# Performance work log

Measured on AMD Instinct MI355X. Metric: run time of the kernel, lower is better.

## Reference

```python
import jax, jax.numpy as jnp
import numpy as np

B, T, D, H = 64, 2048, 128, 256
EPS = 1e-5


def setup_inputs() -> dict:
    key = jax.random.key(0)
    ks = jax.random.split(key, 20)
    s_d = 1.0 / np.sqrt(D)
    s_h = 1.0 / np.sqrt(H)
    s_2h = 1.0 / np.sqrt(2 * H)
    u = lambda k, shape, s: jax.random.uniform(k, shape, jnp.float32, -s, s)
    return {
        "x": jax.random.normal(ks[0], (B, T, D), jnp.float32),
        # gate input projections, stored (in, out)
        "Wi": u(ks[1], (D, H), s_d), "bi": u(ks[2], (H,), s_d),
        "Wf": u(ks[3], (D, H), s_d), "bf": u(ks[4], (H,), s_d),
        "Wc": u(ks[5], (D, H), s_d), "bc": u(ks[6], (H,), s_d),
        "Wo": u(ks[7], (D, H), s_d), "bo": u(ks[8], (H,), s_d),
        # recurrent projections (no bias)
        "Ui": u(ks[9], (H, H), s_h), "Uf": u(ks[10], (H, H), s_h),
        "Uc": u(ks[11], (H, H), s_h), "Uo": u(ks[12], (H, H), s_h),
        # KAN MLP: H -> 2H -> H
        "K1": u(ks[13], (H, 2 * H), s_h), "kb1": u(ks[14], (2 * H,), s_h),
        "K2": u(ks[15], (2 * H, H), s_2h), "kb2": u(ks[16], (H,), s_2h),
        # LayerNorm
        "gamma": jnp.ones((H,), jnp.float32), "beta": jnp.zeros((H,), jnp.float32),
    }


def _layernorm(h, gamma, beta):
    mu = jnp.mean(h, axis=-1, keepdims=True)
    var = jnp.mean(jnp.square(h - mu), axis=-1, keepdims=True)
    return (h - mu) * jax.lax.rsqrt(var + EPS) * gamma + beta


def _forward(x, Wi, bi, Wf, bf, Wc, bc, Wo, bo, Ui, Uf, Uc, Uo, K1, kb1, K2, kb2, gamma, beta):
    # Precompute input projections for all timesteps: (B,T,H) -> scan over T
    xi = jnp.einsum("btd,dh->bth", x, Wi) + bi
    xf = jnp.einsum("btd,dh->bth", x, Wf) + bf
    xc = jnp.einsum("btd,dh->bth", x, Wc) + bc
    xo = jnp.einsum("btd,dh->bth", x, Wo) + bo
    xs = jnp.stack([xi, xf, xc, xo], axis=0).transpose(2, 0, 1, 3)  # (T,4,B,H)

    h0 = jnp.zeros((x.shape[0], Wi.shape[1]), x.dtype)
    c0 = jnp.zeros_like(h0)

    def step(carry, xt):
        h, c = carry
        xi_t, xf_t, xc_t, xo_t = xt[0], xt[1], xt[2], xt[3]
        i_t = jax.nn.sigmoid(xi_t + h @ Ui)
        f_t = jax.nn.sigmoid(xf_t + h @ Uf)
        c_tilde = jnp.tanh(xc_t + h @ Uc)
        o_t = jax.nn.sigmoid(xo_t + h @ Uo)
        c = f_t * c + i_t * c_tilde
        c_tr = jnp.tanh(c @ K1 + kb1) @ K2 + kb2  # KAN transform
        h = o_t * jnp.tanh(c_tr)
        h = _layernorm(h, gamma, beta)  # dropout is identity in eval mode
        return (h, c), h

    (h, c), ys = jax.lax.scan(step, (h0, c0), xs)
    output = ys.transpose(1, 0, 2)  # (B,T,H)
    return output, h, c


def reference(x, Wi, bi, Wf, bf, Wc, bc, Wo, bo, Ui, Uf, Uc, Uo, K1, kb1, K2, kb2, gamma, beta):
    return _forward(x, Wi, bi, Wf, bf, Wc, bc, Wo, bo, Ui, Uf, Uc, Uo, K1, kb1, K2, kb2, gamma, beta)
```

## Files before the change

### kernel.cpp

```cpp
#include <hip/hip_runtime.h>

#define B 64
#define T 2048
#define D 128
#define H 256
#define H2 512
#define NP 4
#define CHUNK 8

#define ROW_U64 1536
#define WS_NEEDED ((size_t)B * ROW_U64 * 8)
#define SPIN_LIM (1 << 20)

__device__ __forceinline__ float sigmoid_f(float x) { return 1.f / (1.f + __expf(-x)); }
__device__ __forceinline__ float tanh_f(float x) {
    float e = __expf(2.f * x);
    return 1.f - 2.f / (e + 1.f);
}
__device__ __forceinline__ unsigned long long pack_tag(float v, unsigned int tag) {
    return ((unsigned long long)tag << 32) | (unsigned long long)__float_as_uint(v);
}
__device__ __forceinline__ float poll_tagged(const unsigned long long* __restrict__ ptr,
                                             unsigned int tag, bool& alive) {
    unsigned long long v;
    if (alive) {
        int cnt = 0;
        do {
            v = __hip_atomic_load(ptr, __ATOMIC_RELAXED, __HIP_MEMORY_SCOPE_AGENT);
            if ((unsigned int)(v >> 32) == tag)
                return __uint_as_float((unsigned int)v);
        } while (++cnt < SPIN_LIM);
        alive = false;
    }
    v = __hip_atomic_load(ptr, __ATOMIC_RELAXED, __HIP_MEMORY_SCOPE_AGENT);
    return __uint_as_float((unsigned int)v);
}

#define FMA4(A_, S_, W_) \
    A_.x = fmaf(S_, W_.x, A_.x); A_.y = fmaf(S_, W_.y, A_.y); \
    A_.z = fmaf(S_, W_.z, A_.z); A_.w = fmaf(S_, W_.w, A_.w);

__global__ __launch_bounds__(512, 2) void scan_kernel(
    const float* __restrict__ x,
    const float* __restrict__ Wi, const float* __restrict__ bi,
    const float* __restrict__ Wf, const float* __restrict__ bf,
    const float* __restrict__ Wc, const float* __restrict__ bc,
    const float* __restrict__ Wo, const float* __restrict__ bo,
    const float* __restrict__ Ui, const float* __restrict__ Uf,
    const float* __restrict__ Uc, const float* __restrict__ Uo,
    const float* __restrict__ K1, const float* __restrict__ kb1,
    const float* __restrict__ K2, const float* __restrict__ kb2,
    const float* __restrict__ gamma, const float* __restrict__ beta,
    float* __restrict__ out,
    unsigned long long* __restrict__ ws)
{
    const int bid = blockIdx.x;
    const int b   = bid >> 2;
    const int p   = bid & 3;
    const int tid = threadIdx.x;

    __shared__ float k2lds[128 * 256];
    __shared__ float xw[CHUNK][256];
    __shared__ float red[2048];
    __shared__ float hs[H], cs[H], os[H], us[H], ts[128];

    const int kq  = tid >> 6;
    const int grp = tid & 63;
    const int gG  = grp >> 4;
    const int jG  = (grp & 15) * 4;
    const int ks1 = ((tid >> 6) << 1) | ((tid >> 5) & 1);
    const int mg1 = tid & 31;

    const float* Ug = (gG == 0) ? Ui : (gG == 1) ? Uf : (gG == 2) ? Uc : Uo;
    const float* Wg = (gG == 0) ? Wi : (gG == 1) ? Wf : (gG == 2) ? Wc : Wo;

    float4 uw[32];
    #pragma unroll
    for (int k = 0; k < 32; ++k)
        uw[k] = *(const float4*)(Ug + (size_t)(kq * 32 + k) * H + p * 64 + jG);

    float4 k1w[16];
    #pragma unroll
    for (int k = 0; k < 16; ++k)
        k1w[k] = *(const float4*)(K1 + (size_t)(ks1 * 16 + k) * H2 + p * 128 + mg1 * 4);

    for (int idx = tid; idx < 128 * 64; idx += 512) {
        int k = idx >> 6, jg = (idx & 63) * 4;
        *(float4*)&k2lds[k * 256 + jg] = *(const float4*)(K2 + (size_t)(p * 128 + k) * H + jg);
    }

    float bcat = 0.f, kb1r = 0.f, kb2r = 0.f;
    float4 gam4, bet4;
    if (tid < 256) {
        const int g = tid >> 6, jj = tid & 63;
        const float* bp = (g == 0) ? bi : (g == 1) ? bf : (g == 2) ? bc : bo;
        bcat = bp[p * 64 + jj];
        kb2r = kb2[tid];
    }
    if (tid < 128) kb1r = kb1[p * 128 + tid];
    if (tid < 64) {
        gam4 = *(const float4*)(gamma + tid * 4);
        bet4 = *(const float4*)(beta + tid * 4);
    }

    if (tid < 256) hs[tid] = 0.f;
    float c_reg = 0.f;

    const float* xrow = x + (size_t)b * T * D;
    float* yb = out + (size_t)b * T * H;
    unsigned long long* rowp  = ws + (size_t)b * ROW_U64;
    unsigned long long* slotC = rowp;
    unsigned long long* slotO = rowp + 256;
    unsigned long long* slotH = rowp + 512;
    const int dqu = __builtin_amdgcn_readfirstlane(kq);

    bool alive = true;
    __syncthreads();

    for (int t = 0; t < T; ++t) {
        const int tt8 = t & (CHUNK - 1);
        const unsigned int seq = (unsigned int)(t + 1);

        if (tt8 == 0) {
            const float* Wp = Wg + p * 64 + jG;
            #pragma unroll
            for (int pass = 0; pass < 2; ++pass) {
                float4 acc[4];
                #pragma unroll
                for (int r = 0; r < 4; ++r) acc[r] = make_float4(0.f, 0.f, 0.f, 0.f);
                #pragma unroll 4
                for (int dd = 0; dd < 16; ++dd) {
                    const int d = dqu * 16 + dd;
                    float4 w = *(const float4*)(Wp + (size_t)d * H);
                    #pragma unroll
                    for (int r = 0; r < 4; ++r) {
                        float xv = xrow[(size_t)(t + pass * 4 + r) * D + d];
                        FMA4(acc[r], xv, w);
                    }
                }
                #pragma unroll
                for (int r = 0; r < 4; ++r) {
                    *(float4*)&red[kq * 256 + grp * 4] = acc[r];
                    __syncthreads();
                    if (tid < 256) {
                        float s = bcat;
                        #pragma unroll
                        for (int q = 0; q < 8; ++q) s += red[q * 256 + tid];
                        xw[pass * 4 + r][tid] = s;
                    }
                    __syncthreads();
                }
            }
        }

        {
            float4 a = make_float4(0.f, 0.f, 0.f, 0.f);
            #pragma unroll
            for (int k4 = 0; k4 < 8; ++k4) {
                float4 hv = *(const float4*)&hs[kq * 32 + k4 * 4];
                FMA4(a, hv.x, uw[k4 * 4 + 0]);
                FMA4(a, hv.y, uw[k4 * 4 + 1]);
                FMA4(a, hv.z, uw[k4 * 4 + 2]);
                FMA4(a, hv.w, uw[k4 * 4 + 3]);
            }
            *(float4*)&red[kq * 256 + grp * 4] = a;
        }
        __syncthreads();
        if (tid < 64) {
            const int j = tid;
            float si = xw[tt8][j],        sf = xw[tt8][64 + j],
                  sg = xw[tt8][128 + j],  so = xw[tt8][192 + j];
            #pragma unroll
            for (int q = 0; q < 8; ++q) {
                si += red[q * 256 + j];
                sf += red[q * 256 + 64 + j];
                sg += red[q * 256 + 128 + j];
                so += red[q * 256 + 192 + j];
            }
            float iv = sigmoid_f(si), fv = sigmoid_f(sf);
            float gv = tanh_f(sg),    ov = sigmoid_f(so);
            float c = fmaf(fv, c_reg, iv * gv);
            c_reg = c;
            cs[p * 64 + j] = c;
            os[p * 64 + j] = ov;
            __hip_atomic_store(slotC + p * 64 + j, pack_tag(c, seq),
                               __ATOMIC_RELAXED, __HIP_MEMORY_SCOPE_AGENT);
            __hip_atomic_store(slotO + p * 64 + j, pack_tag(ov, seq),
                               __ATOMIC_RELAXED, __HIP_MEMORY_SCOPE_AGENT);
        } else if (tid < 448) {
            const int idx = tid - 64;
            if (idx < 192) {
                const int q  = (p + 1 + (idx >> 6)) & 3;
                const int gj = q * 64 + (idx & 63);
                cs[gj] = poll_tagged(slotC + gj, seq, alive);
            } else {
                const int i2 = idx - 192;
                const int q  = (p + 1 + (i2 >> 6)) & 3;
                const int gj = q * 64 + (i2 & 63);
                os[gj] = poll_tagged(slotO + gj, seq, alive);
            }
        }
        __syncthreads();

        {
            float4 a = make_float4(0.f, 0.f, 0.f, 0.f);
            #pragma unroll
            for (int k4 = 0; k4 < 4; ++k4) {
                float4 cv = *(const float4*)&cs[ks1 * 16 + k4 * 4];
                FMA4(a, cv.x, k1w[k4 * 4 + 0]);
                FMA4(a, cv.y, k1w[k4 * 4 + 1]);
                FMA4(a, cv.z, k1w[k4 * 4 + 2]);
                FMA4(a, cv.w, k1w[k4 * 4 + 3]);
            }
            *(float4*)&red[ks1 * 128 + mg1 * 4] = a;
        }
        __syncthreads();
        if (tid < 128) {
            float s = kb1r;
            #pragma unroll
            for (int q = 0; q < 16; ++q) s += red[q * 128 + tid];
            ts[tid] = tanh_f(s);
        }
        __syncthreads();

        {
            float4 a = make_float4(0.f, 0.f, 0.f, 0.f);
            #pragma unroll
            for (int kk = 0; kk < 16; kk += 4) {
                float4 tv = *(const float4*)&ts[kq * 16 + kk];
                float4 w0 = *(const float4*)&k2lds[(kq * 16 + kk + 0) * 256 + grp * 4];
                float4 w1 = *(const float4*)&k2lds[(kq * 16 + kk + 1) * 256 + grp * 4];
                float4 w2 = *(const float4*)&k2lds[(kq * 16 + kk + 2) * 256 + grp * 4];
                float4 w3 = *(const float4*)&k2lds[(kq * 16 + kk + 3) * 256 + grp * 4];
                FMA4(a, tv.x, w0);
                FMA4(a, tv.y, w1);
                FMA4(a, tv.z, w2);
                FMA4(a, tv.w, w3);
            }
            *(float4*)&red[kq * 256 + grp * 4] = a;
        }
        __syncthreads();
        if (tid < 256) {
            float ph = 0.f;
            #pragma unroll
            for (int q = 0; q < 8; ++q) ph += red[q * 256 + tid];
            __hip_atomic_store(slotH + p * 256 + tid, pack_tag(ph, seq),
                               __ATOMIC_RELAXED, __HIP_MEMORY_SCOPE_AGENT);
            const unsigned long long* q1 = slotH + (((p + 1) & 3) << 8) + tid;
            const unsigned long long* q2 = slotH + (((p + 2) & 3) << 8) + tid;
            const unsigned long long* q3 = slotH + (((p + 3) & 3) << 8) + tid;
            unsigned long long v1 = 0, v2 = 0, v3 = 0;
            bool d1 = false, d2 = false, d3 = false;
            int cnt = 0;
            const int lim = alive ? SPIN_LIM : 2;
            while (true) {
                if (!d1) v1 = __hip_atomic_load(q1, __ATOMIC_RELAXED, __HIP_MEMORY_SCOPE_AGENT);
                if (!d2) v2 = __hip_atomic_load(q2, __ATOMIC_RELAXED, __HIP_MEMORY_SCOPE_AGENT);
                if (!d3) v3 = __hip_atomic_load(q3, __ATOMIC_RELAXED, __HIP_MEMORY_SCOPE_AGENT);
                d1 = d1 | ((unsigned int)(v1 >> 32) == seq);
                d2 = d2 | ((unsigned int)(v2 >> 32) == seq);
                d3 = d3 | ((unsigned int)(v3 >> 32) == seq);
                if (d1 & d2 & d3) break;
                if (++cnt > lim) { alive = false; break; }
            }
            float hp = ph + __uint_as_float((unsigned int)v1)
                          + __uint_as_float((unsigned int)v2)
                          + __uint_as_float((unsigned int)v3) + kb2r;
            us[tid] = os[tid] * tanh_f(hp);
        }
        __syncthreads();

        if (tid < 64) {
            float4 u4 = *(const float4*)&us[tid * 4];
            float s1 = u4.x + u4.y + u4.z + u4.w;
            float s2 = u4.x * u4.x + u4.y * u4.y + u4.z * u4.z + u4.w * u4.w;
            #pragma unroll
            for (int off = 32; off > 0; off >>= 1) {
                s1 += __shfl_xor(s1, off);
                s2 += __shfl_xor(s2, off);
            }
            float mu   = s1 * (1.f / 256.f);
            float var  = fmaf(-mu, mu, s2 * (1.f / 256.f));
            float rstd = rsqrtf(var + 1e-5f);
            float4 hn;
            hn.x = (u4.x - mu) * rstd * gam4.x + bet4.x;
            hn.y = (u4.y - mu) * rstd * gam4.y + bet4.y;
            hn.z = (u4.z - mu) * rstd * gam4.z + bet4.z;
            hn.w = (u4.w - mu) * rstd * gam4.w + bet4.w;
            *(float4*)&hs[tid * 4] = hn;
            if ((tid >> 4) == p) {
                *(float4*)(yb + (size_t)t * H + tid * 4) = hn;
                if (t == T - 1) {
                    *(float4*)(out + (size_t)B * T * H + (size_t)b * H + tid * 4) = hn;
                    float4 c4 = *(const float4*)&cs[tid * 4];
                    *(float4*)(out + (size_t)B * T * H + (size_t)B * H + (size_t)b * H + tid * 4) = c4;
                }
            }
        }
        __syncthreads();
    }
}

extern "C" void kernel_launch(void* const* d_in, const int* in_sizes, int n_in,
                              void* d_out, int out_size, void* d_ws, size_t ws_size,
                              hipStream_t stream) {
    (void)in_sizes; (void)n_in; (void)out_size;
    if (ws_size < WS_NEEDED) return;

    const float* x     = (const float*)d_in[0];
    const float* Wi    = (const float*)d_in[1];
    const float* bi    = (const float*)d_in[2];
    const float* Wf    = (const float*)d_in[3];
    const float* bf    = (const float*)d_in[4];
    const float* Wc    = (const float*)d_in[5];
    const float* bc    = (const float*)d_in[6];
    const float* Wo    = (const float*)d_in[7];
    const float* bo    = (const float*)d_in[8];
    const float* Ui    = (const float*)d_in[9];
    const float* Uf    = (const float*)d_in[10];
    const float* Uc    = (const float*)d_in[11];
    const float* Uo    = (const float*)d_in[12];
    const float* K1    = (const float*)d_in[13];
    const float* kb1   = (const float*)d_in[14];
    const float* K2    = (const float*)d_in[15];
    const float* kb2   = (const float*)d_in[16];
    const float* gamma = (const float*)d_in[17];
    const float* beta  = (const float*)d_in[18];
    float* out = (float*)d_out;

    scan_kernel<<<dim3(B * NP), dim3(512), 0, stream>>>(
        x, Wi, bi, Wf, bf, Wc, bc, Wo, bo,
        Ui, Uf, Uc, Uo, K1, kb1, K2, kb2, gamma, beta, out,
        (unsigned long long*)d_ws);
}
```

Baseline: 15.55 ms.

## Process two batch rows per block group to overlap cross-block waits

```diff
diff --git a/kernel.cpp b/kernel.cpp
--- a/kernel.cpp
+++ b/kernel.cpp
@@ -1,15 +1,16 @@
 #include <hip/hip_runtime.h>
 
-#define B 64
+#define NB 64
 #define T 2048
 #define D 128
 #define H 256
 #define H2 512
 #define NP 4
-#define CHUNK 8
+#define PAIRS 32
+#define CHUNK 4
 
 #define ROW_U64 1536
-#define WS_NEEDED ((size_t)B * ROW_U64 * 8)
+#define WS_NEEDED ((size_t)NB * ROW_U64 * 8)
 #define SPIN_LIM (1 << 20)
 
 __device__ __forceinline__ float sigmoid_f(float x) { return 1.f / (1.f + __expf(-x)); }
@@ -54,15 +55,18 @@
     float* __restrict__ out,
     unsigned long long* __restrict__ ws)
 {
-    const int bid = blockIdx.x;
-    const int b   = bid >> 2;
-    const int p   = bid & 3;
-    const int tid = threadIdx.x;
+    const int bid  = blockIdx.x;
+    const int pair = bid >> 2;
+    const int p    = bid & 3;
+    const int tid  = threadIdx.x;
+    const int rowA = pair;
+    const int rowB = pair + PAIRS;
 
     __shared__ float k2lds[128 * 256];
-    __shared__ float xw[CHUNK][256];
-    __shared__ float red[2048];
-    __shared__ float hs[H], cs[H], os[H], us[H], ts[128];
+    __shared__ float xwA[CHUNK][256], xwB[CHUNK][256];
+    __shared__ float red1[2048], red2[2048];
+    __shared__ float hsA[H], hsB[H], csA[H], csB[H], osA[H], osB[H];
+    __shared__ float tsA[128], tsB[128];
 
     const int kq  = tid >> 6;
     const int grp = tid & 63;
@@ -89,67 +93,74 @@
         *(float4*)&k2lds[k * 256 + jg] = *(const float4*)(K2 + (size_t)(p * 128 + k) * H + jg);
     }
 
-    float bcat = 0.f, kb1r = 0.f, kb2r = 0.f;
+    float bcat, kb1r, kb2r = 0.f;
     float4 gam4, bet4;
-    if (tid < 256) {
-        const int g = tid >> 6, jj = tid & 63;
-        const float* bp = (g == 0) ? bi : (g == 1) ? bf : (g == 2) ? bc : bo;
+    {
+        const int col = tid & 255;
+        const int g2 = col >> 6, jj = col & 63;
+        const float* bp = (g2 == 0) ? bi : (g2 == 1) ? bf : (g2 == 2) ? bc : bo;
         bcat = bp[p * 64 + jj];
-        kb2r = kb2[tid];
+        kb1r = kb1[p * 128 + (tid & 127)];
     }
-    if (tid < 128) kb1r = kb1[p * 128 + tid];
+    if (tid < 256) kb2r = kb2[tid];
     if (tid < 64) {
         gam4 = *(const float4*)(gamma + tid * 4);
         bet4 = *(const float4*)(beta + tid * 4);
     }
 
-    if (tid < 256) hs[tid] = 0.f;
-    float c_reg = 0.f;
-
-    const float* xrow = x + (size_t)b * T * D;
-    float* yb = out + (size_t)b * T * H;
-    unsigned long long* rowp  = ws + (size_t)b * ROW_U64;
-    unsigned long long* slotC = rowp;
-    unsigned long long* slotO = rowp + 256;
-    unsigned long long* slotH = rowp + 512;
+    if (tid < 256) { hsA[tid] = 0.f; hsB[tid] = 0.f; }
+    float c_regA = 0.f, c_regB = 0.f;
+
+    const float* xrowA = x + (size_t)rowA * T * D;
+    const float* xrowB = x + (size_t)rowB * T * D;
+    float* ybA = out + (size_t)rowA * T * H;
+    float* ybB = out + (size_t)rowB * T * H;
+    unsigned long long* slotC_A = ws + (size_t)rowA * ROW_U64;
+    unsigned long long* slotO_A = slotC_A + 256;
+    unsigned long long* slotH_A = slotC_A + 512;
+    unsigned long long* slotC_B = ws + (size_t)rowB * ROW_U64;
+    unsigned long long* slotO_B = slotC_B + 256;
+    unsigned long long* slotH_B = slotC_B + 512;
     const int dqu = __builtin_amdgcn_readfirstlane(kq);
 
     bool alive = true;
     __syncthreads();
 
     for (int t = 0; t < T; ++t) {
-        const int tt8 = t & (CHUNK - 1);
+        const int tt4 = t & (CHUNK - 1);
         const unsigned int seq = (unsigned int)(t + 1);
 
-        if (tt8 == 0) {
+        if (tt4 == 0) {
             const float* Wp = Wg + p * 64 + jG;
             #pragma unroll
-            for (int pass = 0; pass < 2; ++pass) {
-                float4 acc[4];
-                #pragma unroll
-                for (int r = 0; r < 4; ++r) acc[r] = make_float4(0.f, 0.f, 0.f, 0.f);
+            for (int r4 = 0; r4 < CHUNK; ++r4) {
+                float4 aA = make_float4(0.f, 0.f, 0.f, 0.f);
+                float4 aB = make_float4(0.f, 0.f, 0.f, 0.f);
                 #pragma unroll 4
                 for (int dd = 0; dd < 16; ++dd) {
                     const int d = dqu * 16 + dd;
                     float4 w = *(const float4*)(Wp + (size_t)d * H);
+                    float xa = xrowA[(size_t)(t + r4) * D + d];
+                    float xb = xrowB[(size_t)(t + r4) * D + d];
+                    FMA4(aA, xa, w);
+                    FMA4(aB, xb, w);
+                }
+                *(float4*)&red1[kq * 256 + grp * 4] = aA;
+                *(float4*)&red2[kq * 256 + grp * 4] = aB;
+                __syncthreads();
+                if (tid < 256) {
+                    float s = bcat;
                     #pragma unroll
-                    for (int r = 0; r < 4; ++r) {
-                        float xv = xrow[(size_t)(t + pass * 4 + r) * D + d];
-                        FMA4(acc[r], xv, w);
-                    }
+                    for (int q = 0; q < 8; ++q) s += red1[q * 256 + tid];
+                    xwA[r4][tid] = s;
+                } else {
+                    const int col = tid - 256;
+                    float s = bcat;
+                    #pragma unroll
+                    for (int q = 0; q < 8; ++q) s += red2[q * 256 + col];
+                    xwB[r4][col] = s;
                 }
-                #pragma unroll
-                for (int r = 0; r < 4; ++r) {
-                    *(float4*)&red[kq * 256 + grp * 4] = acc[r];
-                    __syncthreads();
-                    if (tid < 256) {
-                        float s = bcat;
-                        #pragma unroll
-                        for (int q = 0; q < 8; ++q) s += red[q * 256 + tid];
-                        xw[pass * 4 + r][tid] = s;
-                    }
-                    __syncthreads();
-                }
+                __syncthreads();
             }
         }
 
@@ -157,47 +168,89 @@
             float4 a = make_float4(0.f, 0.f, 0.f, 0.f);
             #pragma unroll
             for (int k4 = 0; k4 < 8; ++k4) {
-                float4 hv = *(const float4*)&hs[kq * 32 + k4 * 4];
+                float4 hv = *(const float4*)&hsA[kq * 32 + k4 * 4];
                 FMA4(a, hv.x, uw[k4 * 4 + 0]);
                 FMA4(a, hv.y, uw[k4 * 4 + 1]);
                 FMA4(a, hv.z, uw[k4 * 4 + 2]);
                 FMA4(a, hv.w, uw[k4 * 4 + 3]);
             }
-            *(float4*)&red[kq * 256 + grp * 4] = a;
-        }
-        __syncthreads();
-        if (tid < 64) {
-            const int j = tid;
-            float si = xw[tt8][j],        sf = xw[tt8][64 + j],
-                  sg = xw[tt8][128 + j],  so = xw[tt8][192 + j];
+            *(float4*)&red1[kq * 256 + grp * 4] = a;
+        }
+        __syncthreads();
+
+        {
+            const int j = tid & 63;
+            float si = xwA[tt4][j],       sf = xwA[tt4][64 + j],
+                  sg = xwA[tt4][128 + j], so = xwA[tt4][192 + j];
             #pragma unroll
             for (int q = 0; q < 8; ++q) {
-                si += red[q * 256 + j];
-                sf += red[q * 256 + 64 + j];
-                sg += red[q * 256 + 128 + j];
-                so += red[q * 256 + 192 + j];
+                si += red1[q * 256 + j];
+                sf += red1[q * 256 + 64 + j];
+                sg += red1[q * 256 + 128 + j];
+                so += red1[q * 256 + 192 + j];
             }
             float iv = sigmoid_f(si), fv = sigmoid_f(sf);
             float gv = tanh_f(sg),    ov = sigmoid_f(so);
-            float c = fmaf(fv, c_reg, iv * gv);
-            c_reg = c;
-            cs[p * 64 + j] = c;
-            os[p * 64 + j] = ov;
-            __hip_atomic_store(slotC + p * 64 + j, pack_tag(c, seq),
-                               __ATOMIC_RELAXED, __HIP_MEMORY_SCOPE_AGENT);
-            __hip_atomic_store(slotO + p * 64 + j, pack_tag(ov, seq),
-                               __ATOMIC_RELAXED, __HIP_MEMORY_SCOPE_AGENT);
-        } else if (tid < 448) {
-            const int idx = tid - 64;
+            float c = fmaf(fv, c_regA, iv * gv);
+            c_regA = c;
+            if (tid >= 448) {
+                csA[p * 64 + j] = c;
+                osA[p * 64 + j] = ov;
+                __hip_atomic_store(slotC_A + p * 64 + j, pack_tag(c, seq),
+                                   __ATOMIC_RELAXED, __HIP_MEMORY_SCOPE_AGENT);
+                __hip_atomic_store(slotO_A + p * 64 + j, pack_tag(ov, seq),
+                                   __ATOMIC_RELAXED, __HIP_MEMORY_SCOPE_AGENT);
+            }
+        }
+        {
+            float4 a = make_float4(0.f, 0.f, 0.f, 0.f);
+            #pragma unroll
+            for (int k4 = 0; k4 < 8; ++k4) {
+                float4 hv = *(const float4*)&hsB[kq * 32 + k4 * 4];
+                FMA4(a, hv.x, uw[k4 * 4 + 0]);
+                FMA4(a, hv.y, uw[k4 * 4 + 1]);
+                FMA4(a, hv.z, uw[k4 * 4 + 2]);
+                FMA4(a, hv.w, uw[k4 * 4 + 3]);
+            }
+            *(float4*)&red2[kq * 256 + grp * 4] = a;
+        }
+        __syncthreads();
+
+        {
+            const int j = tid & 63;
+            float si = xwB[tt4][j],       sf = xwB[tt4][64 + j],
+                  sg = xwB[tt4][128 + j], so = xwB[tt4][192 + j];
+            #pragma unroll
+            for (int q = 0; q < 8; ++q) {
+                si += red2[q * 256 + j];
+                sf += red2[q * 256 + 64 + j];
+                sg += red2[q * 256 + 128 + j];
+                so += red2[q * 256 + 192 + j];
+            }
+            float iv = sigmoid_f(si), fv = sigmoid_f(sf);
+            float gv = tanh_f(sg),    ov = sigmoid_f(so);
+            float c = fmaf(fv, c_regB, iv * gv);
+            c_regB = c;
+            if (tid >= 448) {
+                csB[p * 64 + j] = c;
+                osB[p * 64 + j] = ov;
+                __hip_atomic_store(slotC_B + p * 64 + j, pack_tag(c, seq),
+                                   __ATOMIC_RELAXED, __HIP_MEMORY_SCOPE_AGENT);
+                __hip_atomic_store(slotO_B + p * 64 + j, pack_tag(ov, seq),
+                                   __ATOMIC_RELAXED, __HIP_MEMORY_SCOPE_AGENT);
+            }
+        }
+        if (tid < 384) {
+            const int idx = tid;
             if (idx < 192) {
                 const int q  = (p + 1 + (idx >> 6)) & 3;
                 const int gj = q * 64 + (idx & 63);
-                cs[gj] = poll_tagged(slotC + gj, seq, alive);
+                csA[gj] = poll_tagged(slotC_A + gj, seq, alive);
             } else {
                 const int i2 = idx - 192;
                 const int q  = (p + 1 + (i2 >> 6)) & 3;
                 const int gj = q * 64 + (i2 & 63);
-                os[gj] = poll_tagged(slotO + gj, seq, alive);
+                osA[gj] = poll_tagged(slotO_A + gj, seq, alive);
             }
         }
         __syncthreads();
@@ -206,20 +259,33 @@
             float4 a = make_float4(0.f, 0.f, 0.f, 0.f);
             #pragma unroll
             for (int k4 = 0; k4 < 4; ++k4) {
-                float4 cv = *(const float4*)&cs[ks1 * 16 + k4 * 4];
+                float4 cv = *(const float4*)&csA[ks1 * 16 + k4 * 4];
                 FMA4(a, cv.x, k1w[k4 * 4 + 0]);
                 FMA4(a, cv.y, k1w[k4 * 4 + 1]);
                 FMA4(a, cv.z, k1w[k4 * 4 + 2]);
                 FMA4(a, cv.w, k1w[k4 * 4 + 3]);
             }
-            *(float4*)&red[ks1 * 128 + mg1 * 4] = a;
-        }
-        __syncthreads();
+            *(float4*)&red1[ks1 * 128 + mg1 * 4] = a;
+        }
+        __syncthreads();
+
         if (tid < 128) {
             float s = kb1r;
             #pragma unroll
-            for (int q = 0; q < 16; ++q) s += red[q * 128 + tid];
-            ts[tid] = tanh_f(s);
+            for (int q = 0; q < 16; ++q) s += red1[q * 128 + tid];
+            tsA[tid] = tanh_f(s);
+        } else {
+            const int idx = tid - 128;
+            if (idx < 192) {
+                const int q  = (p + 1 + (idx >> 6)) & 3;
+                const int gj = q * 64 + (idx & 63);
+                csB[gj] = poll_tagged(slotC_B + gj, seq, alive);
+            } else {
+                const int i2 = idx - 192;
+                const int q  = (p + 1 + (i2 >> 6)) & 3;
+                const int gj = q * 64 + (i2 & 63);
+                osB[gj] = poll_tagged(slotO_B + gj, seq, alive);
+            }
         }
         __syncthreads();
 
@@ -227,7 +293,7 @@
             float4 a = make_float4(0.f, 0.f, 0.f, 0.f);
             #pragma unroll
             for (int kk = 0; kk < 16; kk += 4) {
-                float4 tv = *(const float4*)&ts[kq * 16 + kk];
+                float4 tv = *(const float4*)&tsA[kq * 16 + kk];
                 float4 w0 = *(const float4*)&k2lds[(kq * 16 + kk + 0) * 256 + grp * 4];
                 float4 w1 = *(const float4*)&k2lds[(kq * 16 + kk + 1) * 256 + grp * 4];
                 float4 w2 = *(const float4*)&k2lds[(kq * 16 + kk + 2) * 256 + grp * 4];
@@ -237,18 +303,41 @@
                 FMA4(a, tv.z, w2);
                 FMA4(a, tv.w, w3);
             }
-            *(float4*)&red[kq * 256 + grp * 4] = a;
-        }
-        __syncthreads();
+            *(float4*)&red1[kq * 256 + grp * 4] = a;
+        }
+        {
+            float4 a = make_float4(0.f, 0.f, 0.f, 0.f);
+            #pragma unroll
+            for (int k4 = 0; k4 < 4; ++k4) {
+                float4 cv = *(const float4*)&csB[ks1 * 16 + k4 * 4];
+                FMA4(a, cv.x, k1w[k4 * 4 + 0]);
+                FMA4(a, cv.y, k1w[k4 * 4 + 1]);
+                FMA4(a, cv.z, k1w[k4 * 4 + 2]);
+                FMA4(a, cv.w, k1w[k4 * 4 + 3]);
+            }
+            *(float4*)&red2[ks1 * 128 + mg1 * 4] = a;
+        }
+        __syncthreads();
+
+        float phA = 0.f;
         if (tid < 256) {
-            float ph = 0.f;
-            #pragma unroll
-            for (int q = 0; q < 8; ++q) ph += red[q * 256 + tid];
-            __hip_atomic_store(slotH + p * 256 + tid, pack_tag(ph, seq),
+            #pragma unroll
+            for (int q = 0; q < 8; ++q) phA += red1[q * 256 + tid];
+            __hip_atomic_store(slotH_A + p * 256 + tid, pack_tag(phA, seq),
                                __ATOMIC_RELAXED, __HIP_MEMORY_SCOPE_AGENT);
-            const unsigned long long* q1 = slotH + (((p + 1) & 3) << 8) + tid;
-            const unsigned long long* q2 = slotH + (((p + 2) & 3) << 8) + tid;
-            const unsigned long long* q3 = slotH + (((p + 3) & 3) << 8) + tid;
+        } else if (tid < 384) {
+            const int col = tid - 256;
+            float s = kb1r;
+            #pragma unroll
+            for (int q = 0; q < 16; ++q) s += red2[q * 128 + col];
+            tsB[col] = tanh_f(s);
+        }
+        __syncthreads();
+
+        if (tid < 256) {
+            const unsigned long long* q1 = slotH_A + (((p + 1) & 3) << 8) + tid;
+            const unsigned long long* q2 = slotH_A + (((p + 2) & 3) << 8) + tid;
+            const unsigned long long* q3 = slotH_A + (((p + 3) & 3) << 8) + tid;
             unsigned long long v1 = 0, v2 = 0, v3 = 0;
             bool d1 = false, d2 = false, d3 = false;
             int cnt = 0;
@@ -263,15 +352,38 @@
                 if (d1 & d2 & d3) break;
                 if (++cnt > lim) { alive = false; break; }
             }
-            float hp = ph + __uint_as_float((unsigned int)v1)
-                          + __uint_as_float((unsigned int)v2)
-                          + __uint_as_float((unsigned int)v3) + kb2r;
-            us[tid] = os[tid] * tanh_f(hp);
-        }
-        __syncthreads();
-
+            float hp = phA + __uint_as_float((unsigned int)v1)
+                           + __uint_as_float((unsigned int)v2)
+                           + __uint_as_float((unsigned int)v3) + kb2r;
+            red1[tid] = osA[tid] * tanh_f(hp);
+        } else {
+            const int w4 = kq - 4;
+            float4 a = make_float4(0.f, 0.f, 0.f, 0.f);
+            #pragma unroll
+            for (int kk = 0; kk < 32; kk += 4) {
+                float4 tv = *(const float4*)&tsB[w4 * 32 + kk];
+                float4 w0 = *(const float4*)&k2lds[(w4 * 32 + kk + 0) * 256 + grp * 4];
+                float4 w1 = *(const float4*)&k2lds[(w4 * 32 + kk + 1) * 256 + grp * 4];
+                float4 w2 = *(const float4*)&k2lds[(w4 * 32 + kk + 2) * 256 + grp * 4];
+                float4 w3 = *(const float4*)&k2lds[(w4 * 32 + kk + 3) * 256 + grp * 4];
+                FMA4(a, tv.x, w0);
+                FMA4(a, tv.y, w1);
+                FMA4(a, tv.z, w2);
+                FMA4(a, tv.w, w3);
+            }
+            *(float4*)&red2[w4 * 256 + grp * 4] = a;
+        }
+        __syncthreads();
+
+        float phB = 0.f;
+        if (tid < 256) {
+            #pragma unroll
+            for (int q = 0; q < 4; ++q) phB += red2[q * 256 + tid];
+            __hip_atomic_store(slotH_B + p * 256 + tid, pack_tag(phB, seq),
+                               __ATOMIC_RELAXED, __HIP_MEMORY_SCOPE_AGENT);
+        }
         if (tid < 64) {
-            float4 u4 = *(const float4*)&us[tid * 4];
+            float4 u4 = *(const float4*)&red1[tid * 4];
             float s1 = u4.x + u4.y + u4.z + u4.w;
             float s2 = u4.x * u4.x + u4.y * u4.y + u4.z * u4.z + u4.w * u4.w;
             #pragma unroll
@@ -287,13 +399,67 @@
             hn.y = (u4.y - mu) * rstd * gam4.y + bet4.y;
             hn.z = (u4.z - mu) * rstd * gam4.z + bet4.z;
             hn.w = (u4.w - mu) * rstd * gam4.w + bet4.w;
-            *(float4*)&hs[tid * 4] = hn;
+            *(float4*)&hsA[tid * 4] = hn;
             if ((tid >> 4) == p) {
-                *(float4*)(yb + (size_t)t * H + tid * 4) = hn;
+                *(float4*)(ybA + (size_t)t * H + tid * 4) = hn;
                 if (t == T - 1) {
-                    *(float4*)(out + (size_t)B * T * H + (size_t)b * H + tid * 4) = hn;
-                    float4 c4 = *(const float4*)&cs[tid * 4];
-                    *(float4*)(out + (size_t)B * T * H + (size_t)B * H + (size_t)b * H + tid * 4) = c4;
+                    *(float4*)(out + (size_t)NB * T * H + (size_t)rowA * H + tid * 4) = hn;
+                    float4 c4 = *(const float4*)&csA[tid * 4];
+                    *(float4*)(out + (size_t)NB * T * H + (size_t)NB * H + (size_t)rowA * H + tid * 4) = c4;
+                }
+            }
+        }
+        __syncthreads();
+
+        if (tid < 256) {
+            const unsigned long long* q1 = slotH_B + (((p + 1) & 3) << 8) + tid;
+            const unsigned long long* q2 = slotH_B + (((p + 2) & 3) << 8) + tid;
+            const unsigned long long* q3 = slotH_B + (((p + 3) & 3) << 8) + tid;
+            unsigned long long v1 = 0, v2 = 0, v3 = 0;
+            bool d1 = false, d2 = false, d3 = false;
+            int cnt = 0;
+            const int lim = alive ? SPIN_LIM : 2;
+            while (true) {
+                if (!d1) v1 = __hip_atomic_load(q1, __ATOMIC_RELAXED, __HIP_MEMORY_SCOPE_AGENT);
+                if (!d2) v2 = __hip_atomic_load(q2, __ATOMIC_RELAXED, __HIP_MEMORY_SCOPE_AGENT);
+                if (!d3) v3 = __hip_atomic_load(q3, __ATOMIC_RELAXED, __HIP_MEMORY_SCOPE_AGENT);
+                d1 = d1 | ((unsigned int)(v1 >> 32) == seq);
+                d2 = d2 | ((unsigned int)(v2 >> 32) == seq);
+                d3 = d3 | ((unsigned int)(v3 >> 32) == seq);
+                if (d1 & d2 & d3) break;
+                if (++cnt > lim) { alive = false; break; }
+            }
+            float hp = phB + __uint_as_float((unsigned int)v1)
+                           + __uint_as_float((unsigned int)v2)
+                           + __uint_as_float((unsigned int)v3) + kb2r;
+            red1[256 + tid] = osB[tid] * tanh_f(hp);
+        }
+        __syncthreads();
+
+        if (tid < 64) {
+            float4 u4 = *(const float4*)&red1[256 + tid * 4];
+            float s1 = u4.x + u4.y + u4.z + u4.w;
+            float s2 = u4.x * u4.x + u4.y * u4.y + u4.z * u4.z + u4.w * u4.w;
+            #pragma unroll
+            for (int off = 32; off > 0; off >>= 1) {
+                s1 += __shfl_xor(s1, off);
+                s2 += __shfl_xor(s2, off);
+            }
+            float mu   = s1 * (1.f / 256.f);
+            float var  = fmaf(-mu, mu, s2 * (1.f / 256.f));
+            float rstd = rsqrtf(var + 1e-5f);
+            float4 hn;
+            hn.x = (u4.x - mu) * rstd * gam4.x + bet4.x;
+            hn.y = (u4.y - mu) * rstd * gam4.y + bet4.y;
+            hn.z = (u4.z - mu) * rstd * gam4.z + bet4.z;
+            hn.w = (u4.w - mu) * rstd * gam4.w + bet4.w;
+            *(float4*)&hsB[tid * 4] = hn;
+            if ((tid >> 4) == p) {
+                *(float4*)(ybB + (size_t)t * H + tid * 4) = hn;
+                if (t == T - 1) {
+                    *(float4*)(out + (size_t)NB * T * H + (size_t)rowB * H + tid * 4) = hn;
+                    float4 c4 = *(const float4*)&csB[tid * 4];
+                    *(float4*)(out + (size_t)NB * T * H + (size_t)NB * H + (size_t)rowB * H + tid * 4) = c4;
                 }
             }
         }
@@ -328,7 +494,7 @@
     const float* beta  = (const float*)d_in[18];
     float* out = (float*)d_out;
 
-    scan_kernel<<<dim3(B * NP), dim3(512), 0, stream>>>(
+    scan_kernel<<<dim3(PAIRS * NP), dim3(512), 0, stream>>>(
         x, Wi, bi, Wf, bf, Wc, bc, Wo, bo,
         Ui, Uf, Uc, Uo, K1, kb1, K2, kb2, gamma, beta, out,
         (unsigned long long*)d_ws);
```

Measured after the change: 31.23 ms. 2.01x slower.

## Replace LDS reduction passes in KAN matvecs with shuffle-based column-per-thread dot products

Applied to the files above, without the earlier changes.

```diff
diff --git a/kernel.cpp b/kernel.cpp
--- a/kernel.cpp
+++ b/kernel.cpp
@@ -39,6 +39,8 @@
 #define FMA4(A_, S_, W_) \
     A_.x = fmaf(S_, W_.x, A_.x); A_.y = fmaf(S_, W_.y, A_.y); \
     A_.z = fmaf(S_, W_.z, A_.z); A_.w = fmaf(S_, W_.w, A_.w);
+
+#define K2P 132
 
 __global__ __launch_bounds__(512, 2) void scan_kernel(
     const float* __restrict__ x,
@@ -59,7 +61,7 @@
     const int p   = bid & 3;
     const int tid = threadIdx.x;
 
-    __shared__ float k2lds[128 * 256];
+    __shared__ float k2t[256 * K2P];
     __shared__ float xw[CHUNK][256];
     __shared__ float red[2048];
     __shared__ float hs[H], cs[H], os[H], us[H], ts[128];
@@ -68,8 +70,6 @@
     const int grp = tid & 63;
     const int gG  = grp >> 4;
     const int jG  = (grp & 15) * 4;
-    const int ks1 = ((tid >> 6) << 1) | ((tid >> 5) & 1);
-    const int mg1 = tid & 31;
 
     const float* Ug = (gG == 0) ? Ui : (gG == 1) ? Uf : (gG == 2) ? Uc : Uo;
     const float* Wg = (gG == 0) ? Wi : (gG == 1) ? Wf : (gG == 2) ? Wc : Wo;
@@ -79,25 +79,33 @@
     for (int k = 0; k < 32; ++k)
         uw[k] = *(const float4*)(Ug + (size_t)(kq * 32 + k) * H + p * 64 + jG);
 
+    const int c1  = tid >> 2;
+    const int ks  = tid & 3;
     float4 k1w[16];
     #pragma unroll
-    for (int k = 0; k < 16; ++k)
-        k1w[k] = *(const float4*)(K1 + (size_t)(ks1 * 16 + k) * H2 + p * 128 + mg1 * 4);
-
-    for (int idx = tid; idx < 128 * 64; idx += 512) {
-        int k = idx >> 6, jg = (idx & 63) * 4;
-        *(float4*)&k2lds[k * 256 + jg] = *(const float4*)(K2 + (size_t)(p * 128 + k) * H + jg);
-    }
-
-    float bcat = 0.f, kb1r = 0.f, kb2r = 0.f;
+    for (int i = 0; i < 16; ++i) {
+        float4 v;
+        v.x = K1[(size_t)(ks * 64 + i * 4 + 0) * H2 + p * 128 + c1];
+        v.y = K1[(size_t)(ks * 64 + i * 4 + 1) * H2 + p * 128 + c1];
+        v.z = K1[(size_t)(ks * 64 + i * 4 + 2) * H2 + p * 128 + c1];
+        v.w = K1[(size_t)(ks * 64 + i * 4 + 3) * H2 + p * 128 + c1];
+        k1w[i] = v;
+    }
+
+    for (int idx = tid; idx < 128 * 256; idx += 512) {
+        int k = idx >> 8, c = idx & 255;
+        k2t[c * K2P + k] = K2[(size_t)(p * 128 + k) * H + c];
+    }
+
+    float bcat = 0.f;
+    const float kb1r = kb1[p * 128 + c1];
+    const float kb2r = kb2[tid >> 1];
     float4 gam4, bet4;
     if (tid < 256) {
         const int g = tid >> 6, jj = tid & 63;
         const float* bp = (g == 0) ? bi : (g == 1) ? bf : (g == 2) ? bc : bo;
         bcat = bp[p * 64 + jj];
-        kb2r = kb2[tid];
-    }
-    if (tid < 128) kb1r = kb1[p * 128 + tid];
+    }
     if (tid < 64) {
         gam4 = *(const float4*)(gamma + tid * 4);
         bet4 = *(const float4*)(beta + tid * 4);
@@ -166,6 +174,7 @@
             *(float4*)&red[kq * 256 + grp * 4] = a;
         }
         __syncthreads();
+
         if (tid < 64) {
             const int j = tid;
             float si = xw[tt8][j],        sf = xw[tt8][64 + j],
@@ -203,70 +212,54 @@
         __syncthreads();
 
         {
-            float4 a = make_float4(0.f, 0.f, 0.f, 0.f);
-            #pragma unroll
-            for (int k4 = 0; k4 < 4; ++k4) {
-                float4 cv = *(const float4*)&cs[ks1 * 16 + k4 * 4];
-                FMA4(a, cv.x, k1w[k4 * 4 + 0]);
-                FMA4(a, cv.y, k1w[k4 * 4 + 1]);
-                FMA4(a, cv.z, k1w[k4 * 4 + 2]);
-                FMA4(a, cv.w, k1w[k4 * 4 + 3]);
-            }
-            *(float4*)&red[ks1 * 128 + mg1 * 4] = a;
-        }
-        __syncthreads();
-        if (tid < 128) {
-            float s = kb1r;
-            #pragma unroll
-            for (int q = 0; q < 16; ++q) s += red[q * 128 + tid];
-            ts[tid] = tanh_f(s);
+            float a = 0.f;
+            #pragma unroll
+            for (int i = 0; i < 16; ++i) {
+                float4 cv = *(const float4*)&cs[ks * 64 + i * 4];
+                a += cv.x * k1w[i].x + cv.y * k1w[i].y
+                   + cv.z * k1w[i].z + cv.w * k1w[i].w;
+            }
+            a += __shfl_xor(a, 1);
+            a += __shfl_xor(a, 2);
+            if (ks == 0) ts[c1] = tanh_f(a + kb1r);
         }
         __syncthreads();
 
         {
-            float4 a = make_float4(0.f, 0.f, 0.f, 0.f);
-            #pragma unroll
-            for (int kk = 0; kk < 16; kk += 4) {
-                float4 tv = *(const float4*)&ts[kq * 16 + kk];
-                float4 w0 = *(const float4*)&k2lds[(kq * 16 + kk + 0) * 256 + grp * 4];
-                float4 w1 = *(const float4*)&k2lds[(kq * 16 + kk + 1) * 256 + grp * 4];
-                float4 w2 = *(const float4*)&k2lds[(kq * 16 + kk + 2) * 256 + grp * 4];
-                float4 w3 = *(const float4*)&k2lds[(kq * 16 + kk + 3) * 256 + grp * 4];
-                FMA4(a, tv.x, w0);
-                FMA4(a, tv.y, w1);
-                FMA4(a, tv.z, w2);
-                FMA4(a, tv.w, w3);
-            }
-            *(float4*)&red[kq * 256 + grp * 4] = a;
-        }
-        __syncthreads();
-        if (tid < 256) {
-            float ph = 0.f;
-            #pragma unroll
-            for (int q = 0; q < 8; ++q) ph += red[q * 256 + tid];
-            __hip_atomic_store(slotH + p * 256 + tid, pack_tag(ph, seq),
-                               __ATOMIC_RELAXED, __HIP_MEMORY_SCOPE_AGENT);
-            const unsigned long long* q1 = slotH + (((p + 1) & 3) << 8) + tid;
-            const unsigned long long* q2 = slotH + (((p + 2) & 3) << 8) + tid;
-            const unsigned long long* q3 = slotH + (((p + 3) & 3) << 8) + tid;
-            unsigned long long v1 = 0, v2 = 0, v3 = 0;
-            bool d1 = false, d2 = false, d3 = false;
-            int cnt = 0;
-            const int lim = alive ? SPIN_LIM : 2;
-            while (true) {
-                if (!d1) v1 = __hip_atomic_load(q1, __ATOMIC_RELAXED, __HIP_MEMORY_SCOPE_AGENT);
-                if (!d2) v2 = __hip_atomic_load(q2, __ATOMIC_RELAXED, __HIP_MEMORY_SCOPE_AGENT);
-                if (!d3) v3 = __hip_atomic_load(q3, __ATOMIC_RELAXED, __HIP_MEMORY_SCOPE_AGENT);
-                d1 = d1 | ((unsigned int)(v1 >> 32) == seq);
-                d2 = d2 | ((unsigned int)(v2 >> 32) == seq);
-                d3 = d3 | ((unsigned int)(v3 >> 32) == seq);
-                if (d1 & d2 & d3) break;
-                if (++cnt > lim) { alive = false; break; }
-            }
-            float hp = ph + __uint_as_float((unsigned int)v1)
-                          + __uint_as_float((unsigned int)v2)
-                          + __uint_as_float((unsigned int)v3) + kb2r;
-            us[tid] = os[tid] * tanh_f(hp);
+            const int col = tid >> 1, kh = tid & 1;
+            float a = 0.f;
+            #pragma unroll
+            for (int i = 0; i < 16; ++i) {
+                float4 tv = *(const float4*)&ts[kh * 64 + i * 4];
+                float4 wv = *(const float4*)&k2t[col * K2P + kh * 64 + i * 4];
+                a += tv.x * wv.x + tv.y * wv.y + tv.z * wv.z + tv.w * wv.w;
+            }
+            a += __shfl_xor(a, 1);
+            if (kh == 0) {
+                __hip_atomic_store(slotH + p * 256 + col, pack_tag(a, seq),
+                                   __ATOMIC_RELAXED, __HIP_MEMORY_SCOPE_AGENT);
+                const unsigned long long* q1 = slotH + (((p + 1) & 3) << 8) + col;
+                const unsigned long long* q2 = slotH + (((p + 2) & 3) << 8) + col;
+                const unsigned long long* q3 = slotH + (((p + 3) & 3) << 8) + col;
+                unsigned long long v1 = 0, v2 = 0, v3 = 0;
+                bool d1 = false, d2 = false, d3 = false;
+                int cnt = 0;
+                const int lim = alive ? SPIN_LIM : 2;
+                while (true) {
+                    if (!d1) v1 = __hip_atomic_load(q1, __ATOMIC_RELAXED, __HIP_MEMORY_SCOPE_AGENT);
+                    if (!d2) v2 = __hip_atomic_load(q2, __ATOMIC_RELAXED, __HIP_MEMORY_SCOPE_AGENT);
+                    if (!d3) v3 = __hip_atomic_load(q3, __ATOMIC_RELAXED, __HIP_MEMORY_SCOPE_AGENT);
+                    d1 = d1 | ((unsigned int)(v1 >> 32) == seq);
+                    d2 = d2 | ((unsigned int)(v2 >> 32) == seq);
+                    d3 = d3 | ((unsigned int)(v3 >> 32) == seq);
+                    if (d1 & d2 & d3) break;
+                    if (++cnt > lim) { alive = false; break; }
+                }
+                float hp = a + __uint_as_float((unsigned int)v1)
+                             + __uint_as_float((unsigned int)v2)
+                             + __uint_as_float((unsigned int)v3) + kb2r;
+                us[col] = os[col] * tanh_f(hp);
+            }
         }
         __syncthreads();
 
```

Measured after the change: 16.13 ms. +3.7%, slower.
